# Kernel tuning notes

Hardware: AMD Instinct MI355X
Metric: run time of the kernel (lower is better)

Reference implementation:

```python
import jax, jax.numpy as jnp
import numpy as np

DIM = 1024
N_HEADS = 16
HEAD_DIM = DIM // N_HEADS
SCALE = HEAD_DIM ** -0.5


def setup_inputs() -> dict:
    key = jax.random.key(0)
    ks = jax.random.split(key, 5)
    x = jax.random.normal(ks[0], (4, 2048, DIM), dtype=jnp.float32)
    # nn.Linear weights stored as [out, in]; we keep [in, out] for x @ W
    w_qkv = jax.random.normal(ks[1], (DIM, 3 * DIM), dtype=jnp.float32) * (DIM ** -0.5)
    b_qkv = jnp.zeros((3 * DIM,), dtype=jnp.float32)
    w_proj = jax.random.normal(ks[2], (DIM, DIM), dtype=jnp.float32) * (DIM ** -0.5)
    b_proj = jnp.zeros((DIM,), dtype=jnp.float32)
    return {"x": x, "w_qkv": w_qkv, "b_qkv": b_qkv, "w_proj": w_proj, "b_proj": b_proj}


def reference(x, w_qkv, b_qkv, w_proj, b_proj):
    B, S, D = x.shape
    qkv = x @ w_qkv + b_qkv                                   # [B,S,3D]
    qkv = qkv.reshape(B, S, 3, N_HEADS, HEAD_DIM)
    qkv = jnp.transpose(qkv, (2, 0, 3, 1, 4))                 # [3,B,H,S,hd]
    q, k, v = qkv[0], qkv[1], qkv[2]
    attn = jnp.einsum("bhqd,bhkd->bhqk", q, k) * SCALE        # [B,H,S,S]
    attn = jax.nn.softmax(attn, axis=-1)
    out = jnp.einsum("bhqk,bhkd->bhqd", attn, v)              # [B,H,S,hd]
    out = jnp.transpose(out, (0, 2, 1, 3)).reshape(B, S, D)   # [B,S,D]
    return out @ w_proj + b_proj
```

## Files before the change

### kernel.cpp

```cpp
#include <hip/hip_runtime.h>
#include <hip/hip_bf16.h>

typedef float f32x4 __attribute__((ext_vector_type(4)));
typedef short bf16x8 __attribute__((ext_vector_type(8)));
typedef unsigned short ushort8 __attribute__((ext_vector_type(8)));
typedef unsigned int uint2v __attribute__((ext_vector_type(2)));

__device__ __forceinline__ unsigned short f2bf(float f) {
    union { float f; unsigned u; } v; v.f = f;
    unsigned r = v.u + 0x7fffu + ((v.u >> 16) & 1u);
    return (unsigned short)(r >> 16);
}

__device__ __forceinline__ unsigned short f2bf_hw(float f) {
    union { __hip_bfloat16 b; unsigned short u; } cv;
    cv.b = __float2bfloat16(f);
    return cv.u;
}

#define GLDS16(g, l)                                                        \
    __builtin_amdgcn_global_load_lds(                                       \
        (const __attribute__((address_space(1))) unsigned int*)(const void*)(g), \
        (__attribute__((address_space(3))) unsigned int*)(void*)(l), 16, 0, 0)

__global__ __launch_bounds__(256) void k_prep(const float* __restrict__ x,
                                              unsigned short* __restrict__ xb,
                                              const float* __restrict__ wq,
                                              unsigned short* __restrict__ wqt,
                                              const float* __restrict__ wp,
                                              unsigned short* __restrict__ wpt) {
    __shared__ float t[32][33];
    int bid = blockIdx.x, tid = threadIdx.x;
    if (bid < 4096) {
        int i = bid * 256 + tid;
        float4 a = ((const float4*)x)[i * 2];
        float4 b = ((const float4*)x)[i * 2 + 1];
        ushort8 o = { f2bf(a.x), f2bf(a.y), f2bf(a.z), f2bf(a.w),
                      f2bf(b.x), f2bf(b.y), f2bf(b.z), f2bf(b.w) };
        ((ushort8*)xb)[i] = o;
        return;
    }
    const float* in; unsigned short* out; int C, c0, r0;
    const int R = 1024;
    if (bid < 7168) {
        int bx = bid - 4096; in = wq; out = wqt; C = 3072;
        c0 = (bx % 96) * 32; r0 = (bx / 96) * 32;
    } else {
        int bx = bid - 7168; in = wp; out = wpt; C = 1024;
        c0 = (bx & 31) * 32; r0 = (bx >> 5) * 32;
    }
    int tx = tid & 31, ty = tid >> 5;
#pragma unroll
    for (int i = 0; i < 4; i++)
        t[ty + i * 8][tx] = in[(size_t)(r0 + ty + i * 8) * C + c0 + tx];
    __syncthreads();
#pragma unroll
    for (int i = 0; i < 4; i++)
        out[(size_t)(c0 + ty + i * 8) * R + r0 + tx] = f2bf(t[tx][ty + i * 8]);
}

template <int MODE>
__global__ __launch_bounds__(256)
void k_gemm(const unsigned short* __restrict__ A, const unsigned short* __restrict__ Bt,
            const float* __restrict__ bias, int M, int N, int K,
            float* __restrict__ outF, unsigned short* __restrict__ q_ws,
            unsigned short* __restrict__ k_ws, unsigned short* __restrict__ vt_ws) {
    __shared__ __attribute__((aligned(16))) unsigned short SMEM[(MODE == 1) ? 64 * 136
                                                                            : 128 * 64];
    unsigned short* Ash = SMEM;
    unsigned short* Bsh = SMEM + 128 * 32;
    int tid = threadIdx.x;
    int lane = tid & 63, w = tid >> 6;
    int wr = w >> 1, wc = w & 1;

    int nbx = gridDim.x;
    int flat = blockIdx.y * nbx + blockIdx.x;
    int cpx = (nbx * gridDim.y) >> 3;
    int wg = (flat & 7) * cpx + (flat >> 3);
    int m0 = (wg / nbx) * 128, n0 = (wg % nbx) * 128;

    f32x4 acc[4][4] = {};

    int srow = tid >> 2, sk = (tid & 3) * 8;
    const unsigned short* aS0 = A + (size_t)(m0 + srow) * K + sk;
    const unsigned short* aS1 = A + (size_t)(m0 + 64 + srow) * K + sk;
    const unsigned short* bS0 = Bt + (size_t)(n0 + srow) * K + sk;
    const unsigned short* bS1 = Bt + (size_t)(n0 + 64 + srow) * K + sk;
    unsigned short* aD0 = Ash + w * 512;
    unsigned short* aD1 = Ash + 2048 + w * 512;
    unsigned short* bD0 = Bsh + w * 512;
    unsigned short* bD1 = Bsh + 2048 + w * 512;

    int ko = (lane >> 4) * 8;
    int arow = (wr * 64 + (lane & 15)) * 32;
    int brow = (wc * 64 + (lane & 15)) * 32;

    for (int k0 = 0; k0 < K; k0 += 32) {
        GLDS16(aS0, aD0);
        GLDS16(aS1, aD1);
        GLDS16(bS0, bD0);
        GLDS16(bS1, bD1);
        aS0 += 32; aS1 += 32; bS0 += 32; bS1 += 32;
        __syncthreads();
        bf16x8 af[4], bfr[4];
#pragma unroll
        for (int i = 0; i < 4; i++) {
            af[i]  = *(const bf16x8*)&Ash[arow + i * 16 * 32 + ko];
            bfr[i] = *(const bf16x8*)&Bsh[brow + i * 16 * 32 + ko];
        }
#pragma unroll
        for (int i = 0; i < 4; i++)
#pragma unroll
            for (int j = 0; j < 4; j++)
                acc[i][j] = __builtin_amdgcn_mfma_f32_16x16x32_bf16(af[i], bfr[j], acc[i][j], 0, 0, 0);
        __syncthreads();
    }

    int colBase = n0 + wc * 64 + (lane & 15);
    int rowBase = m0 + wr * 64 + ((lane >> 4) << 2);

    if constexpr (MODE == 1) {
        if (n0 >= 2048) {
            unsigned short* Vt = SMEM;
            int l15e = lane & 15;
            int rowrd = tid >> 2, colrd = (tid & 3) * 32;
#pragma unroll
            for (int pass = 0; pass < 2; pass++) {
                __syncthreads();
                if (wc == pass) {
#pragma unroll
                    for (int i = 0; i < 4; i++)
#pragma unroll
                        for (int j = 0; j < 4; j++)
#pragma unroll
                            for (int r = 0; r < 4; r++) {
                                int nl = j * 16 + l15e;
                                int ml = wr * 64 + i * 16 + ((lane >> 4) << 2) + r;
                                Vt[nl * 136 + ml] = f2bf(acc[i][j][r] + bias[n0 + pass * 64 + nl]);
                            }
                }
                __syncthreads();
                int rem = (n0 + pass * 64 + rowrd) & 1023;
                unsigned short* dst = vt_ws
                    + ((size_t)((m0 >> 11) * 16 + (rem >> 6)) * 64 + (rem & 63)) * 2048
                    + (m0 & 2047) + colrd;
                const unsigned short* src = &Vt[rowrd * 136 + colrd];
#pragma unroll
                for (int q2 = 0; q2 < 4; q2++)
                    ((uint4*)dst)[q2] = ((const uint4*)src)[q2];
            }
            return;
        }
    }

#pragma unroll
    for (int i = 0; i < 4; i++)
#pragma unroll
        for (int j = 0; j < 4; j++)
#pragma unroll
            for (int r = 0; r < 4; r++) {
                int m = rowBase + i * 16 + r;
                int n = colBase + j * 16;
                float v = acc[i][j][r] + bias[n];
                if constexpr (MODE == 0) {
                    outF[(size_t)m * N + n] = v;
                } else {
                    int which = n >> 10, rem = n & 1023;
                    int h = rem >> 6, d = rem & 63;
                    int b = m >> 11, s = m & 2047;
                    int bh = b * 16 + h;
                    if (which == 0)
                        q_ws[((size_t)bh * 2048 + s) * 64 + d] = f2bf(v * 0.125f);
                    else
                        k_ws[((size_t)bh * 2048 + s) * 64 + d] = f2bf(v);
                }
            }
}

__global__ __launch_bounds__(256)
void k_attn(const unsigned short* __restrict__ q_ws, const unsigned short* __restrict__ k_ws,
            const unsigned short* __restrict__ vt_ws, unsigned short* __restrict__ o_ws) {
    __shared__ __attribute__((aligned(16))) unsigned short Ksh[64 * 64];
    __shared__ __attribute__((aligned(16))) unsigned short Vsh[64 * 64];
    __shared__ __attribute__((aligned(16))) unsigned short Psh[128 * 72];
    int tid = threadIdx.x, lane = tid & 63, w = tid >> 6;
    int l15 = lane & 15, g = lane >> 4;

    int flat = blockIdx.y * 16 + blockIdx.x;
    int wg = (flat & 7) * 128 + (flat >> 3);
    int bh = wg >> 4;
    int q0 = (wg & 15) * 128;
    int b = bh >> 4, h = bh & 15;

    const unsigned short* qp = q_ws + (size_t)bh * 2048 * 64;
    const unsigned short* kp = k_ws + (size_t)bh * 2048 * 64;
    const unsigned short* vp = vt_ws + (size_t)bh * 64 * 2048;

    int ko = g * 8;
    bf16x8 qf[2][2];
#pragma unroll
    for (int half = 0; half < 2; half++) {
        const unsigned short* qr = qp + (size_t)(q0 + w * 32 + half * 16 + l15) * 64;
        qf[half][0] = *(const bf16x8*)(qr + ko);
        qf[half][1] = *(const bf16x8*)(qr + 32 + ko);
    }

    f32x4 oacc[2][4] = {};
    float lacc[2][4] = {};

    int srow = tid >> 2, squad = tid & 3;
    int ssw = (srow & 7) << 3;
    int sbase = srow * 64;
    int sc0 = (squad * 16) ^ ssw;
    int sc1 = (squad * 16 + 8) ^ ssw;

    int kvrow = (srow & 15) * 4 + (srow >> 4);
    const unsigned short* kNext = kp + (size_t)kvrow * 64 + squad * 16;
    const unsigned short* vNext = vp + (size_t)srow * 2048 + squad * 16;

    uint4 kr0, kr1, vr0, vr1;
#define LOADT()                                                                \
    {                                                                          \
        kr0 = *(const uint4*)kNext; kr1 = *(const uint4*)(kNext + 8);          \
        vr0 = *(const uint4*)vNext; vr1 = *(const uint4*)(vNext + 8);          \
        kNext += 64 * 64; vNext += 64;                                         \
    }
#define STORET()                                                               \
    {                                                                          \
        *(uint4*)&Ksh[sbase + sc0] = kr0;                                      \
        *(uint4*)&Ksh[sbase + sc1] = kr1;                                      \
        *(uint4*)&Vsh[sbase + sc0] = vr0;                                      \
        *(uint4*)&Vsh[sbase + sc1] = vr1;                                      \
    }

    LOADT();

    for (int t = 0; t < 32; t++) {
        STORET();
        __syncthreads();

        f32x4 s[2][4];
        __builtin_amdgcn_s_setprio(1);
#pragma unroll
        for (int ct = 0; ct < 4; ct++) {
            int krow = ct * 16 + l15;
            int ksw = (krow & 7) << 3;
            const unsigned short* kb = &Ksh[krow * 64];
            bf16x8 kb0 = *(const bf16x8*)&kb[ko ^ ksw];
            bf16x8 kb1 = *(const bf16x8*)&kb[(32 + ko) ^ ksw];
#pragma unroll
            for (int half = 0; half < 2; half++) {
                f32x4 sa = {};
                sa = __builtin_amdgcn_mfma_f32_16x16x32_bf16(qf[half][0], kb0, sa, 0, 0, 0);
                sa = __builtin_amdgcn_mfma_f32_16x16x32_bf16(qf[half][1], kb1, sa, 0, 0, 0);
                s[half][ct] = sa;
            }
        }
        __builtin_amdgcn_s_setprio(0);

        if (t < 31) LOADT();

#pragma unroll
        for (int half = 0; half < 2; half++)
#pragma unroll
            for (int r = 0; r < 4; r++) {
                int prow = (w * 32 + half * 16 + 4 * g + r) * 72;
                float p0 = __expf(s[half][0][r]);
                float p1 = __expf(s[half][1][r]);
                float p2 = __expf(s[half][2][r]);
                float p3 = __expf(s[half][3][r]);
                lacc[half][r] += (p0 + p1) + (p2 + p3);
                unsigned int u01, u23;
                asm("v_cvt_pk_bf16_f32 %0, %1, %2" : "=v"(u01) : "v"(p0), "v"(p1));
                asm("v_cvt_pk_bf16_f32 %0, %1, %2" : "=v"(u23) : "v"(p2), "v"(p3));
                uint2v pk; pk.x = u01; pk.y = u23;
                *(uint2v*)&Psh[prow + l15 * 4] = pk;
            }

        __syncthreads();

        bf16x8 pa[2][2];
#pragma unroll
        for (int half = 0; half < 2; half++) {
            int parow = (w * 32 + half * 16 + l15) * 72;
            pa[half][0] = *(const bf16x8*)&Psh[parow + ko];
            pa[half][1] = *(const bf16x8*)&Psh[parow + 32 + ko];
        }
        __builtin_amdgcn_s_setprio(1);
#pragma unroll
        for (int ct = 0; ct < 4; ct++) {
            int vrow = ct * 16 + l15;
            int vsw = (vrow & 7) << 3;
            const unsigned short* vb = &Vsh[vrow * 64];
            bf16x8 vb0 = *(const bf16x8*)&vb[ko ^ vsw];
            bf16x8 vb1 = *(const bf16x8*)&vb[(32 + ko) ^ vsw];
#pragma unroll
            for (int half = 0; half < 2; half++) {
                oacc[half][ct] = __builtin_amdgcn_mfma_f32_16x16x32_bf16(pa[half][0], vb0, oacc[half][ct], 0, 0, 0);
                oacc[half][ct] = __builtin_amdgcn_mfma_f32_16x16x32_bf16(pa[half][1], vb1, oacc[half][ct], 0, 0, 0);
            }
        }
        __builtin_amdgcn_s_setprio(0);

        __syncthreads();
    }
#undef LOADT
#undef STORET

#pragma unroll
    for (int half = 0; half < 2; half++)
#pragma unroll
        for (int r = 0; r < 4; r++) {
            float lf = lacc[half][r];
#pragma unroll
            for (int off = 8; off; off >>= 1) lf += __shfl_xor(lf, off);
            float inv = 1.0f / lf;
            int srw = q0 + w * 32 + half * 16 + 4 * g + r;
#pragma unroll
            for (int ct = 0; ct < 4; ct++) {
                int d = ct * 16 + l15;
                o_ws[((size_t)(b * 2048 + srw) * 16 + h) * 64 + d] = f2bf_hw(oacc[half][ct][r] * inv);
            }
        }
}

extern "C" void kernel_launch(void* const* d_in, const int* in_sizes, int n_in,
                              void* d_out, int out_size, void* d_ws, size_t ws_size,
                              hipStream_t stream) {
    const float* x      = (const float*)d_in[0];
    const float* w_qkv  = (const float*)d_in[1];
    const float* b_qkv  = (const float*)d_in[2];
    const float* w_proj = (const float*)d_in[3];
    const float* b_proj = (const float*)d_in[4];
    float* out = (float*)d_out;

    char* ws = (char*)d_ws;
    unsigned short* xb  = (unsigned short*)(ws);
    unsigned short* wqt = (unsigned short*)(ws + 16777216);
    unsigned short* wpt = (unsigned short*)(ws + 23068672);
    unsigned short* qw  = (unsigned short*)(ws + 25165824);
    unsigned short* kw  = (unsigned short*)(ws + 41943040);
    unsigned short* vtw = (unsigned short*)(ws + 58720256);
    unsigned short* ow  = (unsigned short*)(ws + 75497472);

    k_prep<<<8192, 256, 0, stream>>>(x, xb, w_qkv, wqt, w_proj, wpt);
    k_gemm<1><<<dim3(24, 64), 256, 0, stream>>>(xb, wqt, b_qkv, 8192, 3072, 1024,
                                                nullptr, qw, kw, vtw);
    k_attn<<<dim3(16, 64), 256, 0, stream>>>(qw, kw, vtw, ow);
    k_gemm<0><<<dim3(8, 64), 256, 0, stream>>>(ow, wpt, b_proj, 8192, 1024, 1024,
                                               out, nullptr, nullptr, nullptr);
}
```

Measured before the change: 231.4 us.

## Double-buffer K/V tiles in attention using direct global-to-LDS loads

```diff
diff --git a/kernel.cpp b/kernel.cpp
--- a/kernel.cpp
+++ b/kernel.cpp
@@ -180,8 +180,8 @@
 __global__ __launch_bounds__(256)
 void k_attn(const unsigned short* __restrict__ q_ws, const unsigned short* __restrict__ k_ws,
             const unsigned short* __restrict__ vt_ws, unsigned short* __restrict__ o_ws) {
-    __shared__ __attribute__((aligned(16))) unsigned short Ksh[64 * 64];
-    __shared__ __attribute__((aligned(16))) unsigned short Vsh[64 * 64];
+    __shared__ __attribute__((aligned(16))) unsigned short Ksh[2][64 * 64];
+    __shared__ __attribute__((aligned(16))) unsigned short Vsh[2][64 * 64];
     __shared__ __attribute__((aligned(16))) unsigned short Psh[128 * 72];
     int tid = threadIdx.x, lane = tid & 63, w = tid >> 6;
     int l15 = lane & 15, g = lane >> 4;
@@ -208,36 +208,29 @@
     f32x4 oacc[2][4] = {};
     float lacc[2][4] = {};
 
-    int srow = tid >> 2, squad = tid & 3;
-    int ssw = (srow & 7) << 3;
-    int sbase = srow * 64;
-    int sc0 = (squad * 16) ^ ssw;
-    int sc1 = (squad * 16 + 8) ^ ssw;
-
-    int kvrow = (srow & 15) * 4 + (srow >> 4);
-    const unsigned short* kNext = kp + (size_t)kvrow * 64 + squad * 16;
-    const unsigned short* vNext = vp + (size_t)srow * 2048 + squad * 16;
-
-    uint4 kr0, kr1, vr0, vr1;
-#define LOADT()                                                                \
+    int srow8 = tid >> 3;
+    int scol = ((tid & 7) ^ (srow8 & 7)) * 8;
+    int kv0 = (srow8 & 15) * 4 + (srow8 >> 4);
+    const unsigned short* kN0 = kp + (size_t)kv0 * 64 + scol;
+    const unsigned short* kN1 = kp + (size_t)(kv0 + 2) * 64 + scol;
+    const unsigned short* vN0 = vp + (size_t)srow8 * 2048 + scol;
+    const unsigned short* vN1 = vp + (size_t)(srow8 + 32) * 2048 + scol;
+
+#define STAGE(BUF)                                                             \
     {                                                                          \
-        kr0 = *(const uint4*)kNext; kr1 = *(const uint4*)(kNext + 8);          \
-        vr0 = *(const uint4*)vNext; vr1 = *(const uint4*)(vNext + 8);          \
-        kNext += 64 * 64; vNext += 64;                                         \
-    }
-#define STORET()                                                               \
-    {                                                                          \
-        *(uint4*)&Ksh[sbase + sc0] = kr0;                                      \
-        *(uint4*)&Ksh[sbase + sc1] = kr1;                                      \
-        *(uint4*)&Vsh[sbase + sc0] = vr0;                                      \
-        *(uint4*)&Vsh[sbase + sc1] = vr1;                                      \
-    }
-
-    LOADT();
+        GLDS16(kN0, &Ksh[BUF][w * 512]);                                       \
+        GLDS16(kN1, &Ksh[BUF][2048 + w * 512]);                                \
+        GLDS16(vN0, &Vsh[BUF][w * 512]);                                       \
+        GLDS16(vN1, &Vsh[BUF][2048 + w * 512]);                                \
+        kN0 += 4096; kN1 += 4096; vN0 += 64; vN1 += 64;                        \
+    }
+
+    STAGE(0);
+    __syncthreads();
 
     for (int t = 0; t < 32; t++) {
-        STORET();
-        __syncthreads();
+        int cur = t & 1;
+        if (t < 31) STAGE(cur ^ 1);
 
         f32x4 s[2][4];
         __builtin_amdgcn_s_setprio(1);
@@ -245,7 +238,7 @@
         for (int ct = 0; ct < 4; ct++) {
             int krow = ct * 16 + l15;
             int ksw = (krow & 7) << 3;
-            const unsigned short* kb = &Ksh[krow * 64];
+            const unsigned short* kb = &Ksh[cur][krow * 64];
             bf16x8 kb0 = *(const bf16x8*)&kb[ko ^ ksw];
             bf16x8 kb1 = *(const bf16x8*)&kb[(32 + ko) ^ ksw];
 #pragma unroll
@@ -257,8 +250,6 @@
             }
         }
         __builtin_amdgcn_s_setprio(0);
-
-        if (t < 31) LOADT();
 
 #pragma unroll
         for (int half = 0; half < 2; half++)
@@ -291,7 +282,7 @@
         for (int ct = 0; ct < 4; ct++) {
             int vrow = ct * 16 + l15;
             int vsw = (vrow & 7) << 3;
-            const unsigned short* vb = &Vsh[vrow * 64];
+            const unsigned short* vb = &Vsh[cur][vrow * 64];
             bf16x8 vb0 = *(const bf16x8*)&vb[ko ^ vsw];
             bf16x8 vb1 = *(const bf16x8*)&vb[(32 + ko) ^ vsw];
 #pragma unroll
@@ -304,8 +295,7 @@
 
         __syncthreads();
     }
-#undef LOADT
-#undef STORET
+#undef STAGE
 
 #pragma unroll
     for (int half = 0; half < 2; half++)
```

Result: no change. 230.1 us (-0.6%).
